# Kernel optimization log

Hardware: AMD Instinct MI355X
Metric: run time of the kernel (lower is better)

The kernel has to match this reference:

```python
import jax, jax.numpy as jnp
import numpy as np

D_MODEL = 1024
NUM_HEADS = 16
THRESHOLD = 0.1
B, L, S = 4, 2048, 2048


def setup_inputs() -> dict:
    key = jax.random.key(0)
    ks = jax.random.split(key, 12)
    scale = 0.02
    inp = {
        "q_x": jax.random.normal(ks[0], (B, L, D_MODEL), jnp.float32),
        "k_x": jax.random.normal(ks[1], (B, S, D_MODEL), jnp.float32),
        "v_x": jax.random.normal(ks[2], (B, S, D_MODEL), jnp.float32),
        "energy_coeffs": jax.random.normal(ks[3], (B, S, 1), jnp.float32),
        "Wq": jax.random.normal(ks[4], (D_MODEL, D_MODEL), jnp.float32) * scale,
        "bq": jnp.zeros((D_MODEL,), jnp.float32),
        "Wk": jax.random.normal(ks[5], (D_MODEL, D_MODEL), jnp.float32) * scale,
        "bk": jnp.zeros((D_MODEL,), jnp.float32),
        "Wv": jax.random.normal(ks[6], (D_MODEL, D_MODEL), jnp.float32) * scale,
        "bv": jnp.zeros((D_MODEL,), jnp.float32),
        "Wo": jax.random.normal(ks[7], (D_MODEL, D_MODEL), jnp.float32) * scale,
        "bo": jnp.zeros((D_MODEL,), jnp.float32),
    }
    return inp


def reference(q_x, k_x, v_x, energy_coeffs, Wq, bq, Wk, bk, Wv, bv, Wo, bo):
    Bq, Lq, D = q_x.shape
    H = NUM_HEADS
    Dh = D // H
    # projections (torch Linear: x @ W.T + b; here W stored pre-transposed as [D, D])
    Q = (q_x @ Wq + bq).reshape(Bq, Lq, H, Dh).transpose(0, 2, 1, 3)  # [B,H,L,Dh]
    K = (k_x @ Wk + bk).reshape(Bq, -1, H, Dh).transpose(0, 2, 1, 3)  # [B,H,S,Dh]
    V = (v_x @ Wv + bv).reshape(Bq, -1, H, Dh).transpose(0, 2, 1, 3)  # [B,H,S,Dh]
    scores = jnp.einsum("bhld,bhsd->bhls", Q, K) / np.float32(np.sqrt(Dh))
    # per-key energy mask (hard branch: threshold is a python float)
    energy = jnp.abs(energy_coeffs).mean(axis=-1)  # [B,S]
    mask = energy > THRESHOLD  # [B,S]
    scores = jnp.where(mask[:, None, None, :], scores, -jnp.inf)
    attn = jax.nn.softmax(scores, axis=-1)
    attn = jnp.nan_to_num(attn, nan=0.0)
    out = jnp.einsum("bhls,bhsd->bhld", attn, V)  # [B,H,L,Dh]
    out = out.transpose(0, 2, 1, 3).reshape(Bq, Lq, D)
    return out @ Wo + bo
```

## Files before the change

kernel.cpp:

```cpp
#include <hip/hip_runtime.h>
#include <hip/hip_bf16.h>

typedef __attribute__((ext_vector_type(8))) short short8;
typedef __attribute__((ext_vector_type(4))) short short4v;
typedef __attribute__((ext_vector_type(4))) float f32x4;

static __device__ __forceinline__ unsigned short f2bf(float f) {
  unsigned int u = __float_as_uint(f);
  u += 0x7fffu + ((u >> 16) & 1u);
  return (unsigned short)(u >> 16);
}

static __device__ __forceinline__ unsigned cvtpk(float a, float b) {
  unsigned r;
  asm("v_cvt_pk_bf16_f32 %0, %1, %2" : "=v"(r) : "v"(a), "v"(b));
  return r;
}

static __device__ __forceinline__ void gload_lds16(const unsigned short* g,
                                                   unsigned short* l) {
  __builtin_amdgcn_global_load_lds((const __attribute__((address_space(1))) void*)g,
                                   (__attribute__((address_space(3))) void*)l, 16, 0, 0);
}

__global__ void wtrans4_kernel(const float* __restrict__ W0, const float* __restrict__ W1,
                               const float* __restrict__ W2, const float* __restrict__ W3,
                               unsigned short* __restrict__ T0, unsigned short* __restrict__ T1,
                               unsigned short* __restrict__ T2, unsigned short* __restrict__ T3) {
  const float* W = blockIdx.z == 0 ? W0 : (blockIdx.z == 1 ? W1 : (blockIdx.z == 2 ? W2 : W3));
  unsigned short* Wt = blockIdx.z == 0 ? T0 : (blockIdx.z == 1 ? T1 : (blockIdx.z == 2 ? T2 : T3));
  __shared__ float t[32][33];
  int n0 = blockIdx.x * 32, k0 = blockIdx.y * 32;
#pragma unroll
  for (int j = 0; j < 4; ++j)
    t[threadIdx.y + j * 8][threadIdx.x] =
        W[(size_t)(k0 + threadIdx.y + j * 8) * 1024 + n0 + threadIdx.x];
  __syncthreads();
#pragma unroll
  for (int j = 0; j < 4; ++j)
    Wt[(size_t)(n0 + threadIdx.y + j * 8) * 1024 + k0 + threadIdx.x] =
        f2bf(t[threadIdx.x][threadIdx.y + j * 8]);
}

__global__ void mask_kernel(const float* __restrict__ e, float* __restrict__ Mf,
                            unsigned short* __restrict__ Mbf, int n) {
  int i = blockIdx.x * blockDim.x + threadIdx.x;
  if (i < n) {
    float m = (fabsf(e[i]) > 0.1f) ? 1.0f : 0.0f;
    Mf[i] = m;
    Mbf[i] = f2bf(m);
  }
}

template <int SWAP>
__global__ __launch_bounds__(256, 4) void gemm_qkv_kernel(
    const float* __restrict__ Xq32, const float* __restrict__ Xk32,
    const float* __restrict__ Xv32, const unsigned short* __restrict__ Wtq,
    const unsigned short* __restrict__ Wtk, const unsigned short* __restrict__ Wtv,
    const float* __restrict__ bq, const float* __restrict__ bk, const float* __restrict__ bv,
    unsigned short* __restrict__ Qh, unsigned short* __restrict__ Kh,
    unsigned short* __restrict__ Vt, const float* __restrict__ Mf, float c2) {
  const int K = 1024;
  __shared__ unsigned short Al[2][128 * 32];
  __shared__ unsigned short Bl[2][128 * 32];
  const int z = SWAP ? blockIdx.z : 2;
  const float* X32 = SWAP ? (blockIdx.z == 0 ? Xq32 : Xk32) : Xv32;
  const unsigned short* Wt = SWAP ? (blockIdx.z == 0 ? Wtq : Wtk) : Wtv;
  const float* bias = SWAP ? (blockIdx.z == 0 ? bq : bk) : bv;
  const int m0 = blockIdx.x * 128, n0 = blockIdx.y * 128;
  const int tid = threadIdx.x, lane = tid & 63, wid = tid >> 6;
  const int wr = wid >> 1, wc = wid & 1;
  const int g = lane >> 4, lr = lane & 15;
  const f32x4 fz = {0.f, 0.f, 0.f, 0.f};
  f32x4 acc[4][4];
#pragma unroll
  for (int i = 0; i < 4; i++)
#pragma unroll
    for (int j = 0; j < 4; j++) acc[i][j] = fz;

  const int sr0 = tid >> 2;
  const int sr1 = (256 + tid) >> 2;
  const int chk = ((tid & 3) ^ ((tid >> 3) & 3)) * 8;
  const int offr = (g ^ ((lr >> 1) & 3)) * 8;
  const float* pA0 = X32 + (size_t)(m0 + sr0) * K + chk;
  const float* pA1 = X32 + (size_t)(m0 + sr1) * K + chk;

  float4 ra0, ra1, rb0, rb1;

  auto stageB = [&](int kk, int buf) {
    gload_lds16(Wt + (size_t)(n0 + sr0) * K + kk + chk, &Bl[buf][wid * 512]);
    gload_lds16(Wt + (size_t)(n0 + sr1) * K + kk + chk, &Bl[buf][2048 + wid * 512]);
  };
  auto loadA = [&](int kk) {
    ra0 = *(const float4*)(pA0 + kk);
    ra1 = *(const float4*)(pA0 + kk + 4);
    rb0 = *(const float4*)(pA1 + kk);
    rb1 = *(const float4*)(pA1 + kk + 4);
  };
  auto writeA = [&](int buf) {
    uint4 s0, s1;
    s0.x = cvtpk(ra0.x, ra0.y); s0.y = cvtpk(ra0.z, ra0.w);
    s0.z = cvtpk(ra1.x, ra1.y); s0.w = cvtpk(ra1.z, ra1.w);
    s1.x = cvtpk(rb0.x, rb0.y); s1.y = cvtpk(rb0.z, rb0.w);
    s1.z = cvtpk(rb1.x, rb1.y); s1.w = cvtpk(rb1.z, rb1.w);
    *(uint4*)(&Al[buf][tid * 8]) = s0;
    *(uint4*)(&Al[buf][2048 + tid * 8]) = s1;
  };

  loadA(0);
  writeA(0);
  stageB(0, 0);
  loadA(32);
  __syncthreads();

  int buf = 0;
  for (int k0 = 0; k0 < K; k0 += 32) {
    if (k0 < K - 32) {
      writeA(buf ^ 1);
      stageB(k0 + 32, buf ^ 1);
      if (k0 < K - 64) loadA(k0 + 64);
    }
    short8 a[4], b[4];
#pragma unroll
    for (int i = 0; i < 4; i++)
      a[i] = *(const short8*)(&Al[buf][(wr * 64 + i * 16 + lr) * 32 + offr]);
#pragma unroll
    for (int i = 0; i < 4; i++)
      b[i] = *(const short8*)(&Bl[buf][(wc * 64 + i * 16 + lr) * 32 + offr]);
#pragma unroll
    for (int i = 0; i < 4; i++)
#pragma unroll
      for (int j = 0; j < 4; j++) {
        if (SWAP)
          acc[i][j] = __builtin_amdgcn_mfma_f32_16x16x32_bf16(b[j], a[i], acc[i][j], 0, 0, 0);
        else
          acc[i][j] = __builtin_amdgcn_mfma_f32_16x16x32_bf16(a[i], b[j], acc[i][j], 0, 0, 0);
      }
    __syncthreads();
    buf ^= 1;
  }

  if (SWAP) {
    const float scale = (z == 0) ? c2 : 1.0f;
    unsigned short* out = z == 0 ? Qh : Kh;
#pragma unroll
    for (int i = 0; i < 4; i++) {
      const int mrow = m0 + wr * 64 + i * 16 + lr;
      const int b_ = mrow >> 11, l = mrow & 2047;
#pragma unroll
      for (int j = 0; j < 4; j++) {
        const int ncol0 = n0 + wc * 64 + j * 16 + g * 4;
        const int h = ncol0 >> 6, dh = ncol0 & 63;
        const f32x4 bb = *(const f32x4*)(bias + ncol0);
        uint2 st;
        st.x = cvtpk((acc[i][j][0] + bb[0]) * scale, (acc[i][j][1] + bb[1]) * scale);
        st.y = cvtpk((acc[i][j][2] + bb[2]) * scale, (acc[i][j][3] + bb[3]) * scale);
        *(uint2*)(out + ((size_t)(b_ * 16 + h) * 2048 + l) * 64 + dh) = st;
      }
    }
  } else {
#pragma unroll
    for (int i = 0; i < 4; i++) {
      const int mrow0 = m0 + wr * 64 + i * 16 + g * 4;
      const int b_ = mrow0 >> 11, s = mrow0 & 2047;
      const f32x4 mf = *(const f32x4*)(Mf + mrow0);
#pragma unroll
      for (int j = 0; j < 4; j++) {
        const int ncol = n0 + wc * 64 + j * 16 + lr;
        const float bv_ = bias[ncol];
        const int h = ncol >> 6, d = ncol & 63;
        uint2 pk;
        pk.x = cvtpk((acc[i][j][0] + bv_) * mf[0], (acc[i][j][1] + bv_) * mf[1]);
        pk.y = cvtpk((acc[i][j][2] + bv_) * mf[2], (acc[i][j][3] + bv_) * mf[3]);
        *(uint2*)(Vt + ((size_t)(b_ * 16 + h) * 64 + d) * 2048 + s) = pk;
      }
    }
  }
}

__global__ __launch_bounds__(256, 4) void gemm_out_kernel(
    const unsigned short* __restrict__ X, const unsigned short* __restrict__ Wt,
    const float* __restrict__ bias, float* __restrict__ out) {
  const int K = 1024;
  __shared__ unsigned short Al[2][128 * 32];
  __shared__ unsigned short Bl[2][128 * 32];
  const int m0 = blockIdx.x * 128, n0 = blockIdx.y * 128;
  const int tid = threadIdx.x, lane = tid & 63, wid = tid >> 6;
  const int wr = wid >> 1, wc = wid & 1;
  const int g = lane >> 4, lr = lane & 15;
  const f32x4 fz = {0.f, 0.f, 0.f, 0.f};
  f32x4 acc[4][4];
#pragma unroll
  for (int i = 0; i < 4; i++)
#pragma unroll
    for (int j = 0; j < 4; j++) acc[i][j] = fz;

  const int sr0 = tid >> 2;
  const int sr1 = (256 + tid) >> 2;
  const int sc0s = ((tid & 3) ^ ((tid >> 3) & 3)) * 8;
  const int offr = (g ^ ((lr >> 1) & 3)) * 8;

  auto stage = [&](int kk, int buf) {
    gload_lds16(X + (size_t)(m0 + sr0) * K + kk + sc0s, &Al[buf][wid * 512]);
    gload_lds16(X + (size_t)(m0 + sr1) * K + kk + sc0s, &Al[buf][2048 + wid * 512]);
    gload_lds16(Wt + (size_t)(n0 + sr0) * K + kk + sc0s, &Bl[buf][wid * 512]);
    gload_lds16(Wt + (size_t)(n0 + sr1) * K + kk + sc0s, &Bl[buf][2048 + wid * 512]);
  };

  stage(0, 0);
  __syncthreads();

  int buf = 0;
  for (int k0 = 0; k0 < K; k0 += 32) {
    if (k0 < K - 32) stage(k0 + 32, buf ^ 1);
    short8 a[4], b[4];
#pragma unroll
    for (int i = 0; i < 4; i++)
      a[i] = *(const short8*)(&Al[buf][(wr * 64 + i * 16 + lr) * 32 + offr]);
#pragma unroll
    for (int i = 0; i < 4; i++)
      b[i] = *(const short8*)(&Bl[buf][(wc * 64 + i * 16 + lr) * 32 + offr]);
#pragma unroll
    for (int i = 0; i < 4; i++)
#pragma unroll
      for (int j = 0; j < 4; j++)
        acc[i][j] = __builtin_amdgcn_mfma_f32_16x16x32_bf16(b[j], a[i], acc[i][j], 0, 0, 0);
    __syncthreads();
    buf ^= 1;
  }

#pragma unroll
  for (int i = 0; i < 4; i++) {
    const int mrow = m0 + wr * 64 + i * 16 + lr;
#pragma unroll
    for (int j = 0; j < 4; j++) {
      const int ncol0 = n0 + wc * 64 + j * 16 + g * 4;
      const f32x4 bb = *(const f32x4*)(bias + ncol0);
      f32x4 st = acc[i][j] + bb;
      *(f32x4*)(out + (size_t)mrow * 1024 + ncol0) = st;
    }
  }
}

__global__ __launch_bounds__(256, 4) void attn_kernel(
    const unsigned short* __restrict__ Qh, const unsigned short* __restrict__ Kh,
    const unsigned short* __restrict__ Vt, const unsigned short* __restrict__ Mbf,
    unsigned short* __restrict__ AO) {
  const int S = 2048;
  __shared__ unsigned short Lds[2][8192];
  int bx = blockIdx.x;
  int lid = (bx & 7) * 128 + (bx >> 3);
  const int bh = lid >> 4, qbb = lid & 15;
  const int b_ = bh >> 4, h = bh & 15;
  const unsigned short* Qp = Qh + (size_t)bh * S * 64;
  const unsigned short* Kp = Kh + (size_t)bh * S * 64;
  const unsigned short* Vp = Vt + (size_t)bh * 64 * S;
  const unsigned short* Mp = Mbf + b_ * S;
  const int tid = threadIdx.x, lane = tid & 63, wid = tid >> 6;
  const int g = lane >> 4, lr = lane & 15;
  const int qbase = qbb * 128 + wid * 32;
  const f32x4 fz = {0.f, 0.f, 0.f, 0.f};

  const int srow = (lane >> 3);
  const int schk = (lane & 7) ^ srow;
  const int kr0 = wid * 16 + srow, kr1 = wid * 16 + 8 + srow;
  const int pir0 = (kr0 & 32) | ((kr0 & 12) << 1) | ((kr0 & 16) >> 2) | (kr0 & 3);
  const int pir1 = (kr1 & 32) | ((kr1 & 12) << 1) | ((kr1 & 16) >> 2) | (kr1 & 3);
  const unsigned short* gK0 = Kp + (size_t)pir0 * 64 + schk * 8;
  const unsigned short* gK1 = Kp + (size_t)pir1 * 64 + schk * 8;
  const unsigned short* gV0 = Vp + (size_t)kr0 * S + schk * 8;
  const unsigned short* gV1 = Vp + (size_t)kr1 * S + schk * 8;

  const int s7 = lr & 7;
  const int off0 = ((g ^ s7) * 8);
  const int off1 = (((4 + g) ^ s7) * 8);

  short8 qf[2][2];
#pragma unroll
  for (int qt = 0; qt < 2; qt++)
#pragma unroll
    for (int kh = 0; kh < 2; kh++)
      qf[qt][kh] = *(const short8*)(Qp + (size_t)(qbase + qt * 16 + lr) * 64 + kh * 32 + g * 8);

  f32x4 o[2][4];
  f32x4 psA[2];
#pragma unroll
  for (int qt = 0; qt < 2; qt++) {
    psA[qt] = fz;
#pragma unroll
    for (int t = 0; t < 4; t++) o[qt][t] = fz;
  }

  auto stage = [&](int s0, int buf) {
    gload_lds16(gK0 + (size_t)s0 * 64, &Lds[buf][wid * 1024]);
    gload_lds16(gK1 + (size_t)s0 * 64, &Lds[buf][wid * 1024 + 512]);
    gload_lds16(gV0 + s0, &Lds[buf][4096 + wid * 1024]);
    gload_lds16(gV1 + s0, &Lds[buf][4096 + wid * 1024 + 512]);
  };

  stage(0, 0);
  __syncthreads();

  int cur = 0;
  for (int t = 0; t < 32; ++t) {
    const int s0 = t * 64;
    if (t < 31) stage(s0 + 64, cur ^ 1);
    const unsigned short* Kb = &Lds[cur][lr * 64];
    const unsigned short* Vb = &Lds[cur][4096 + lr * 64];

    short8 kf[4][2];
#pragma unroll
    for (int st = 0; st < 4; st++) {
      kf[st][0] = *(const short8*)(Kb + st * 1024 + off0);
      kf[st][1] = *(const short8*)(Kb + st * 1024 + off1);
    }
    short8 mk0 = *(const short8*)(Mp + s0 + g * 8);
    short8 mk1 = *(const short8*)(Mp + s0 + 32 + g * 8);

    union { unsigned u[8]; short8 s8[2]; } pk[2];
    __builtin_amdgcn_s_setprio(1);
#pragma unroll
    for (int qt = 0; qt < 2; qt++) {
#pragma unroll
      for (int st = 0; st < 4; st++) {
        f32x4 a0 = __builtin_amdgcn_mfma_f32_16x16x32_bf16(kf[st][0], qf[qt][0], fz, 0, 0, 0);
        f32x4 s = __builtin_amdgcn_mfma_f32_16x16x32_bf16(kf[st][1], qf[qt][1], a0, 0, 0, 0);
        f32x4 p;
#pragma unroll
        for (int e = 0; e < 4; e++) p[e] = __builtin_amdgcn_exp2f(s[e]);
        pk[qt].u[st * 2] = cvtpk(p[0], p[1]);
        pk[qt].u[st * 2 + 1] = cvtpk(p[2], p[3]);
      }
      psA[qt] = __builtin_amdgcn_mfma_f32_16x16x32_bf16(mk0, pk[qt].s8[0], psA[qt], 0, 0, 0);
      psA[qt] = __builtin_amdgcn_mfma_f32_16x16x32_bf16(mk1, pk[qt].s8[1], psA[qt], 0, 0, 0);
    }
    __builtin_amdgcn_s_setprio(0);

#pragma unroll
    for (int tt = 0; tt < 4; tt++) {
      short8 v0 = *(const short8*)(Vb + tt * 1024 + off0);
      short8 v1 = *(const short8*)(Vb + tt * 1024 + off1);
      __builtin_amdgcn_s_setprio(1);
#pragma unroll
      for (int qt = 0; qt < 2; qt++) {
        o[qt][tt] = __builtin_amdgcn_mfma_f32_16x16x32_bf16(v0, pk[qt].s8[0], o[qt][tt], 0, 0, 0);
        o[qt][tt] = __builtin_amdgcn_mfma_f32_16x16x32_bf16(v1, pk[qt].s8[1], o[qt][tt], 0, 0, 0);
      }
      __builtin_amdgcn_s_setprio(0);
    }
    __syncthreads();
    cur ^= 1;
  }

#pragma unroll
  for (int qt = 0; qt < 2; qt++) {
    float l = psA[qt][0];
    float inv = l > 0.f ? 1.f / l : 0.f;
    size_t row = (size_t)b_ * 2048 + qbase + qt * 16 + lr;
#pragma unroll
    for (int tt = 0; tt < 4; tt++) {
      uint2 wv;
      wv.x = cvtpk(o[qt][tt][0] * inv, o[qt][tt][1] * inv);
      wv.y = cvtpk(o[qt][tt][2] * inv, o[qt][tt][3] * inv);
      *(uint2*)(AO + row * 1024 + h * 64 + tt * 16 + g * 4) = wv;
    }
  }
}

extern "C" void kernel_launch(void* const* d_in, const int* in_sizes, int n_in,
                              void* d_out, int out_size, void* d_ws, size_t ws_size,
                              hipStream_t stream) {
  const float* q_x = (const float*)d_in[0];
  const float* k_x = (const float*)d_in[1];
  const float* v_x = (const float*)d_in[2];
  const float* energy = (const float*)d_in[3];
  const float* Wq = (const float*)d_in[4];
  const float* bq = (const float*)d_in[5];
  const float* Wk = (const float*)d_in[6];
  const float* bk = (const float*)d_in[7];
  const float* Wv = (const float*)d_in[8];
  const float* bv = (const float*)d_in[9];
  const float* Wo = (const float*)d_in[10];
  const float* bo = (const float*)d_in[11];

  char* w = (char*)d_ws;
  auto take = [&](size_t bytes) {
    char* p = w;
    w += (bytes + 255) & ~(size_t)255;
    return p;
  };
  const size_t XB = (size_t)8192 * 1024 * 2;
  unsigned short* Wtq = (unsigned short*)take((size_t)1024 * 1024 * 2);
  unsigned short* Wtk = (unsigned short*)take((size_t)1024 * 1024 * 2);
  unsigned short* Wtv = (unsigned short*)take((size_t)1024 * 1024 * 2);
  unsigned short* Wto = (unsigned short*)take((size_t)1024 * 1024 * 2);
  float* Mf = (float*)take((size_t)8192 * 4);
  unsigned short* Mbf = (unsigned short*)take((size_t)8192 * 2);
  unsigned short* Qh = (unsigned short*)take(XB);
  unsigned short* Kh = (unsigned short*)take(XB);
  unsigned short* Vt = (unsigned short*)take(XB);
  unsigned short* AO = (unsigned short*)take(XB);

  const float c2 = 0.18033688011f;
  wtrans4_kernel<<<dim3(32, 32, 4), dim3(32, 8), 0, stream>>>(Wq, Wk, Wv, Wo, Wtq, Wtk, Wtv, Wto);
  mask_kernel<<<32, 256, 0, stream>>>(energy, Mf, Mbf, 8192);

  gemm_qkv_kernel<1><<<dim3(64, 8, 2), 256, 0, stream>>>(q_x, k_x, v_x, Wtq, Wtk, Wtv,
                                                         bq, bk, bv, Qh, Kh, Vt, Mf, c2);
  gemm_qkv_kernel<0><<<dim3(64, 8, 1), 256, 0, stream>>>(q_x, k_x, v_x, Wtq, Wtk, Wtv,
                                                         bq, bk, bv, Qh, Kh, Vt, Mf, c2);
  attn_kernel<<<1024, 256, 0, stream>>>(Qh, Kh, Vt, Mbf, AO);
  gemm_out_kernel<<<dim3(64, 8), 256, 0, stream>>>(AO, Wto, bo, (float*)d_out);
}
```

Before: 196.8 us.

## Triple-buffer weight tiles in QKV GEMM and relax per-iteration barrier

Gives the B (weight) tiles of the QKV projection GEMM a third shared-memory buffer so async global-to-LDS loads run two k-steps ahead instead of one. The full __syncthreads is replaced by an LDS-only waitcnt plus raw s_barrier, so outstanding global loads are not drained every iteration. The aim is to hide more global-load latency behind MFMA work. The cost is 8KB more LDS per block, which may cut occupancy, and correctness now depends on the implicit vmcnt waits from the A register loads.

```diff
diff --git a/kernel.cpp b/kernel.cpp
--- a/kernel.cpp
+++ b/kernel.cpp
@@ -62,7 +62,7 @@
     unsigned short* __restrict__ Vt, const float* __restrict__ Mf, float c2) {
   const int K = 1024;
   __shared__ unsigned short Al[2][128 * 32];
-  __shared__ unsigned short Bl[2][128 * 32];
+  __shared__ unsigned short Bl[3][128 * 32];
   const int z = SWAP ? blockIdx.z : 2;
   const float* X32 = SWAP ? (blockIdx.z == 0 ? Xq32 : Xk32) : Xv32;
   const unsigned short* Wt = SWAP ? (blockIdx.z == 0 ? Wtq : Wtk) : Wtv;
@@ -87,9 +87,9 @@
 
   float4 ra0, ra1, rb0, rb1;
 
-  auto stageB = [&](int kk, int buf) {
-    gload_lds16(Wt + (size_t)(n0 + sr0) * K + kk + chk, &Bl[buf][wid * 512]);
-    gload_lds16(Wt + (size_t)(n0 + sr1) * K + kk + chk, &Bl[buf][2048 + wid * 512]);
+  auto stageB = [&](int kk, int bi) {
+    gload_lds16(Wt + (size_t)(n0 + sr0) * K + kk + chk, &Bl[bi][wid * 512]);
+    gload_lds16(Wt + (size_t)(n0 + sr1) * K + kk + chk, &Bl[bi][2048 + wid * 512]);
   };
   auto loadA = [&](int kk) {
     ra0 = *(const float4*)(pA0 + kk);
@@ -97,36 +97,39 @@
     rb0 = *(const float4*)(pA1 + kk);
     rb1 = *(const float4*)(pA1 + kk + 4);
   };
-  auto writeA = [&](int buf) {
+  auto writeA = [&](int ai) {
     uint4 s0, s1;
     s0.x = cvtpk(ra0.x, ra0.y); s0.y = cvtpk(ra0.z, ra0.w);
     s0.z = cvtpk(ra1.x, ra1.y); s0.w = cvtpk(ra1.z, ra1.w);
     s1.x = cvtpk(rb0.x, rb0.y); s1.y = cvtpk(rb0.z, rb0.w);
     s1.z = cvtpk(rb1.x, rb1.y); s1.w = cvtpk(rb1.z, rb1.w);
-    *(uint4*)(&Al[buf][tid * 8]) = s0;
-    *(uint4*)(&Al[buf][2048 + tid * 8]) = s1;
+    *(uint4*)(&Al[ai][tid * 8]) = s0;
+    *(uint4*)(&Al[ai][2048 + tid * 8]) = s1;
   };
 
   loadA(0);
+  stageB(0, 0);
   writeA(0);
-  stageB(0, 0);
+  stageB(32, 1);
   loadA(32);
   __syncthreads();
 
-  int buf = 0;
-  for (int k0 = 0; k0 < K; k0 += 32) {
-    if (k0 < K - 32) {
-      writeA(buf ^ 1);
-      stageB(k0 + 32, buf ^ 1);
-      if (k0 < K - 64) loadA(k0 + 64);
+  int ab = 0;
+  int b0 = 0, b1 = 1, b2 = 2;
+  for (int t = 0; t < 32; ++t) {
+    const int k0 = t * 32;
+    if (t < 31) writeA(ab ^ 1);
+    if (t < 30) {
+      stageB(k0 + 64, b2);
+      loadA(k0 + 64);
     }
     short8 a[4], b[4];
 #pragma unroll
     for (int i = 0; i < 4; i++)
-      a[i] = *(const short8*)(&Al[buf][(wr * 64 + i * 16 + lr) * 32 + offr]);
-#pragma unroll
-    for (int i = 0; i < 4; i++)
-      b[i] = *(const short8*)(&Bl[buf][(wc * 64 + i * 16 + lr) * 32 + offr]);
+      a[i] = *(const short8*)(&Al[ab][(wr * 64 + i * 16 + lr) * 32 + offr]);
+#pragma unroll
+    for (int i = 0; i < 4; i++)
+      b[i] = *(const short8*)(&Bl[b0][(wc * 64 + i * 16 + lr) * 32 + offr]);
 #pragma unroll
     for (int i = 0; i < 4; i++)
 #pragma unroll
@@ -136,8 +139,11 @@
         else
           acc[i][j] = __builtin_amdgcn_mfma_f32_16x16x32_bf16(a[i], b[j], acc[i][j], 0, 0, 0);
       }
-    __syncthreads();
-    buf ^= 1;
+    asm volatile("s_waitcnt lgkmcnt(0)" ::: "memory");
+    __builtin_amdgcn_s_barrier();
+    __builtin_amdgcn_sched_barrier(0);
+    ab ^= 1;
+    int tmp = b0; b0 = b1; b1 = b2; b2 = tmp;
   }
 
   if (SWAP) {
```

After: 194.9 us (median of 3 runs). Within noise of the previous version (-1.0%).
